# Kernel optimization log

Measured on AMD Instinct MI355X. Metric: run time of the kernel, lower is better.

The kernel has to match this reference:

```python
import jax, jax.numpy as jnp
import numpy as np

EMB = 1024
HEADS = 16
HEAD_SIZE = EMB // HEADS


def setup_inputs() -> dict:
    key = jax.random.key(0)
    ks = jax.random.split(key, 10)
    s = 1.0 / np.sqrt(EMB)
    return {
        "x": jax.random.normal(ks[0], (2, 2048, EMB), dtype=jnp.float32),
        "ln_gamma": jnp.ones((EMB,), jnp.float32),
        "ln_beta": jnp.zeros((EMB,), jnp.float32),
        "Wq": jax.random.normal(ks[1], (EMB, EMB), jnp.float32) * s,
        "bq": jnp.zeros((EMB,), jnp.float32),
        "Wk": jax.random.normal(ks[2], (EMB, EMB), jnp.float32) * s,
        "bk": jnp.zeros((EMB,), jnp.float32),
        "Wv": jax.random.normal(ks[3], (EMB, EMB), jnp.float32) * s,
        "bv": jnp.zeros((EMB,), jnp.float32),
        "Wo": jax.random.normal(ks[4], (EMB, EMB), jnp.float32) * s,
        "bo": jnpps if False else jnp.zeros((EMB,), jnp.float32),
    }


def _layernorm(x, gamma, beta, eps=1e-5):
    mu = jnp.mean(x, axis=-1, keepdims=True)
    var = jnp.mean(jnp.square(x - mu), axis=-1, keepdims=True)
    return (x - mu) * jax.lax.rsqrt(var + eps) * gamma + beta


def reference(x, ln_gamma, ln_beta, Wq, bq, Wk, bk, Wv, bv, Wo, bo):
    B, L, D = x.shape
    h = _layernorm(x, ln_gamma, ln_beta)
    # projections -> [B, H, L, hd]
    def split_heads(t):
        return t.reshape(B, L, HEADS, HEAD_SIZE).transpose(0, 2, 1, 3)
    q = split_heads(h @ Wq.T + bq)
    k = split_heads(h @ Wk.T + bk)
    v = split_heads(h @ Wv.T + bv)
    scale = HEAD_SIZE ** (-0.5)
    w = jnp.einsum("bhqd,bhkd->bhqk", q, k) * scale  # [B,H,L,L]
    w = jax.nn.softmax(w, axis=-1)
    o = jnp.einsum("bhqk,bhkd->bhqd", w, v)
    o = o.transpose(0, 2, 1, 3).reshape(B, L, D)
    o = o @ Wo.T + bo
    return x + o
```

## Files before the change

kernel.cpp:

```cpp
#include <hip/hip_runtime.h>
#include <math.h>

#define B_   2
#define L_   2048
#define EMB_ 1024
#define H_   16
#define HD_  64
#define M_   (B_ * L_)
#define KSPLIT 4
#define LOG2E 1.44269504088896f

typedef __bf16 bf16x8 __attribute__((ext_vector_type(8)));
typedef __bf16 bf16x4 __attribute__((ext_vector_type(4)));
typedef __bf16 bf16x2 __attribute__((ext_vector_type(2)));
typedef float floatx16 __attribute__((ext_vector_type(16)));
typedef unsigned int uintx2 __attribute__((ext_vector_type(2)));

typedef __attribute__((address_space(1))) const void GV;
typedef __attribute__((address_space(3))) void LV;

#define MFMA32(a, b, c) __builtin_amdgcn_mfma_f32_32x32x16_bf16((a), (b), (c), 0, 0, 0)

#if __has_builtin(__builtin_amdgcn_exp2f)
#define EXP2(x) __builtin_amdgcn_exp2f(x)
#else
#define EXP2(x) exp2f(x)
#endif

#define SWZ(row) ((((row) & 7) ^ (((row) >> 3) & 3)))

__device__ __forceinline__ int pkbf(float a, float b) {
#if __has_builtin(__builtin_amdgcn_cvt_pk_bf16_f32)
    union { bf16x2 v; int i; } u;
    u.v = __builtin_amdgcn_cvt_pk_bf16_f32(a, b);
    return u.i;
#else
    union { __bf16 h[2]; int i; } u;
    u.h[0] = (__bf16)a; u.h[1] = (__bf16)b;
    return u.i;
#endif
}

__global__ __launch_bounds__(256) void cvt_w_kernel(
        const float* __restrict__ s0, const float* __restrict__ s1,
        const float* __restrict__ s2, const float* __restrict__ s3,
        __bf16* __restrict__ d0, __bf16* __restrict__ d1,
        __bf16* __restrict__ d2, __bf16* __restrict__ d3) {
    int z = blockIdx.y;
    const float* s = (z == 0) ? s0 : (z == 1) ? s1 : (z == 2) ? s2 : s3;
    __bf16* d = (z == 0) ? d0 : (z == 1) ? d1 : (z == 2) ? d2 : d3;
    size_t base = (size_t)(blockIdx.x * 256 + threadIdx.x) * 16;
#pragma unroll
    for (int j = 0; j < 4; ++j) {
        float4 f = *(const float4*)(s + base + j * 4);
        bf16x4 t;
        t[0] = (__bf16)f.x; t[1] = (__bf16)f.y; t[2] = (__bf16)f.z; t[3] = (__bf16)f.w;
        *(bf16x4*)(d + base + j * 4) = t;
    }
}

__global__ __launch_bounds__(256) void ln_kernel(
        const float* __restrict__ x, const float* __restrict__ gamma,
        const float* __restrict__ beta, __bf16* __restrict__ h) {
    int row = blockIdx.x;
    int tid = threadIdx.x;
    const float* xr = x + (size_t)row * EMB_;
    float4 v = *(const float4*)(xr + tid * 4);
    float s  = v.x + v.y + v.z + v.w;
    float ss = v.x * v.x + v.y * v.y + v.z * v.z + v.w * v.w;
    for (int off = 32; off; off >>= 1) {
        s  += __shfl_down(s, off, 64);
        ss += __shfl_down(ss, off, 64);
    }
    __shared__ float s1[4], s2[4];
    int wid = tid >> 6;
    if ((tid & 63) == 0) { s1[wid] = s; s2[wid] = ss; }
    __syncthreads();
    if (tid == 0) {
        float a = s1[0] + s1[1] + s1[2] + s1[3];
        float b = s2[0] + s2[1] + s2[2] + s2[3];
        float mu = a / EMB_;
        float var = b / EMB_ - mu * mu;
        s1[0] = mu;
        s2[0] = rsqrtf(var + 1e-5f);
    }
    __syncthreads();
    float mu = s1[0], rstd = s2[0];
    float4 g4 = *(const float4*)(gamma + tid * 4);
    float4 b4 = *(const float4*)(beta + tid * 4);
    bf16x4 o;
    o[0] = (__bf16)((v.x - mu) * rstd * g4.x + b4.x);
    o[1] = (__bf16)((v.y - mu) * rstd * g4.y + b4.y);
    o[2] = (__bf16)((v.z - mu) * rstd * g4.z + b4.z);
    o[3] = (__bf16)((v.w - mu) * rstd * g4.w + b4.w);
    *(bf16x4*)(h + (size_t)row * EMB_ + tid * 4) = o;
}

__device__ __forceinline__ void stage_tile128(const __bf16* gbase, __bf16* lds,
                                              int wave, int lane) {
    int srow = lane >> 3;
    int gch0 = lane & 7;
#pragma unroll
    for (int s = 0; s < 4; ++s) {
        int seg = wave * 4 + s;
        int row = seg * 8 + srow;
        int g = gch0 ^ SWZ(row);
        __builtin_amdgcn_global_load_lds(
            (GV*)(gbase + (size_t)row * EMB_ + g * 8),
            (LV*)(lds + seg * 512 + lane * 8), 16, 0, 0);
    }
}

__global__ __launch_bounds__(256) void gemm_qkv_mfma(
        const __bf16* __restrict__ A, const __bf16* __restrict__ W,
        const float* __restrict__ bq, const float* __restrict__ bk,
        const float* __restrict__ bv,
        __bf16* __restrict__ Qo, __bf16* __restrict__ Ko,
        __bf16* __restrict__ Vto) {
    __shared__ __bf16 As[128 * 64];
    __shared__ __bf16 Bs[128 * 64];
    int tid = threadIdx.x, wave = tid >> 6, lane = tid & 63;
    int wm = wave >> 1, wn = wave & 1;
    int quad = lane >> 5, lq = lane & 31;
    int bm = blockIdx.y * 128, bn = blockIdx.x * 128;

    floatx16 acc[2][2];
#pragma unroll
    for (int i = 0; i < 2; ++i)
#pragma unroll
        for (int j = 0; j < 2; ++j)
#pragma unroll
            for (int r = 0; r < 16; ++r) acc[i][j][r] = 0.f;

    for (int k0 = 0; k0 < EMB_; k0 += 64) {
        __syncthreads();
        stage_tile128(A + (size_t)bm * EMB_ + k0, As, wave, lane);
        stage_tile128(W + (size_t)bn * EMB_ + k0, Bs, wave, lane);
        __syncthreads();
#pragma unroll
        for (int s = 0; s < 4; ++s) {
            int g = 2 * s + quad;
            int r0 = wm * 64 + lq, r1 = r0 + 32;
            int c0 = wn * 64 + lq, c1 = c0 + 32;
            bf16x8 a0 = *(const bf16x8*)&As[r0 * 64 + ((g ^ SWZ(r0)) * 8)];
            bf16x8 a1 = *(const bf16x8*)&As[r1 * 64 + ((g ^ SWZ(r1)) * 8)];
            bf16x8 b0 = *(const bf16x8*)&Bs[c0 * 64 + ((g ^ SWZ(c0)) * 8)];
            bf16x8 b1 = *(const bf16x8*)&Bs[c1 * 64 + ((g ^ SWZ(c1)) * 8)];
            acc[0][0] = MFMA32(a0, b0, acc[0][0]);
            acc[0][1] = MFMA32(a0, b1, acc[0][1]);
            acc[1][0] = MFMA32(a1, b0, acc[1][0]);
            acc[1][1] = MFMA32(a1, b1, acc[1][1]);
        }
    }

#pragma unroll
    for (int mb = 0; mb < 2; ++mb) {
#pragma unroll
        for (int nb = 0; nb < 2; ++nb) {
            int col = bn + wn * 64 + nb * 32 + lq;
            int z = col >> 10;
            int cc = col & 1023;
            float bv_ = (z == 0) ? bq[cc] : (z == 1) ? bk[cc] : bv[cc];
            if (z < 2) {
                __bf16* dst = (z == 0) ? Qo : Ko;
                float qs = (z == 0) ? 0.125f * LOG2E : 1.0f;
#pragma unroll
                for (int r = 0; r < 16; ++r) {
                    int row = bm + wm * 64 + mb * 32 + (r & 3) + 8 * (r >> 2) + 4 * quad;
                    dst[(size_t)row * EMB_ + cc] = (__bf16)((acc[mb][nb][r] + bv_) * qs);
                }
            } else {
                int hh = cc >> 6, d = cc & 63;
#pragma unroll
                for (int rb = 0; rb < 4; ++rb) {
                    int row = bm + wm * 64 + mb * 32 + 8 * rb + 4 * quad;
                    int b = row >> 11, l = row & (L_ - 1);
                    bf16x4 t;
#pragma unroll
                    for (int a = 0; a < 4; ++a) t[a] = (__bf16)(acc[mb][nb][4 * rb + a] + bv_);
                    *(bf16x4*)(Vto + ((size_t)(b * H_ + hh) * HD_ + d) * L_ + l) = t;
                }
            }
        }
    }
}

template <int SEGS>
__device__ __forceinline__ void stage_tile(const __bf16* gbase, __bf16* lds,
                                           int wave, int lane) {
    int srow = lane >> 3;
    int gch0 = lane & 7;
#pragma unroll
    for (int s = 0; s < SEGS; ++s) {
        int seg = wave * SEGS + s;
        int row = seg * 8 + srow;
        int g = gch0 ^ SWZ(row);
        __builtin_amdgcn_global_load_lds(
            (GV*)(gbase + (size_t)row * EMB_ + g * 8),
            (LV*)(lds + seg * 512 + lane * 8), 16, 0, 0);
    }
}

__global__ __launch_bounds__(256) void gemm_out_mfma(
        const __bf16* __restrict__ A, const __bf16* __restrict__ W,
        const float* __restrict__ bias, const float* __restrict__ x,
        float* __restrict__ out) {
    __shared__ __bf16 As[64 * 64];
    __shared__ __bf16 Bs[128 * 64];
    int tid = threadIdx.x, wave = tid >> 6, lane = tid & 63;
    int quad = lane >> 5, lq = lane & 31;
    int bm = blockIdx.y * 64, bn = blockIdx.x * 128;

    floatx16 acc[2];
#pragma unroll
    for (int i = 0; i < 2; ++i)
#pragma unroll
        for (int r = 0; r < 16; ++r) acc[i][r] = 0.f;

    for (int k0 = 0; k0 < EMB_; k0 += 64) {
        __syncthreads();
        stage_tile<2>(A + (size_t)bm * EMB_ + k0, As, wave, lane);
        stage_tile<4>(W + (size_t)bn * EMB_ + k0, Bs, wave, lane);
        __syncthreads();
#pragma unroll
        for (int s = 0; s < 4; ++s) {
            int g = 2 * s + quad;
            int r0 = lq, r1 = lq + 32;
            int c = wave * 32 + lq;
            bf16x8 a0 = *(const bf16x8*)&As[r0 * 64 + ((g ^ SWZ(r0)) * 8)];
            bf16x8 a1 = *(const bf16x8*)&As[r1 * 64 + ((g ^ SWZ(r1)) * 8)];
            bf16x8 b  = *(const bf16x8*)&Bs[c * 64 + ((g ^ SWZ(c)) * 8)];
            acc[0] = MFMA32(a0, b, acc[0]);
            acc[1] = MFMA32(a1, b, acc[1]);
        }
    }

    int col = bn + wave * 32 + lq;
    float bv_ = bias[col];
#pragma unroll
    for (int mb = 0; mb < 2; ++mb) {
#pragma unroll
        for (int r = 0; r < 16; ++r) {
            size_t row = bm + mb * 32 + (r & 3) + 8 * (r >> 2) + 4 * quad;
            out[row * EMB_ + col] = acc[mb][r] + bv_ + x[row * EMB_ + col];
        }
    }
}

__global__ __launch_bounds__(512, 4) void attn_mfma(
        const __bf16* __restrict__ Q,
        const __bf16* __restrict__ K,
        const __bf16* __restrict__ Vt,
        __bf16* __restrict__ Op,
        float* __restrict__ Lp) {
    __shared__ __bf16 Ks[2][64 * 64];
    __shared__ __bf16 Vs[2][64 * 64];

    int tid = threadIdx.x, wave = tid >> 6, lane = tid & 63;
    int quad = lane >> 5, lq = lane & 31;
    int bh = blockIdx.x;
    int ks = blockIdx.z;
    int b = bh >> 4, h = bh & 15;
    int q0 = blockIdx.y * 256 + wave * 32;
    const size_t tok0 = (size_t)b * L_;

    const __bf16* Kb = K + tok0 * EMB_ + h * HD_;
    const __bf16* Vb = Vt + (size_t)bh * HD_ * L_;

    bf16x8 qf[4];
    {
        const __bf16* qp = Q + (tok0 + q0 + lq) * EMB_ + h * HD_ + quad * 8;
#pragma unroll
        for (int s = 0; s < 4; ++s) qf[s] = *(const bf16x8*)(qp + s * 16);
    }

    floatx16 oacc[2];
#pragma unroll
    for (int j = 0; j < 2; ++j)
#pragma unroll
        for (int r = 0; r < 16; ++r) oacc[j][r] = 0.f;
    float lacc = 0.f;

    int srow = lane >> 3, gch0 = lane & 7;

    auto stage = [&](int buf, int kt) {
        int row = wave * 8 + srow;
        int g = gch0 ^ SWZ(row);
        __builtin_amdgcn_global_load_lds(
            (GV*)(Kb + (size_t)(kt + row) * EMB_ + g * 8),
            (LV*)(&Ks[buf][wave * 512 + lane * 8]), 16, 0, 0);
        __builtin_amdgcn_global_load_lds(
            (GV*)(Vb + (size_t)row * L_ + kt + g * 8),
            (LV*)(&Vs[buf][wave * 512 + lane * 8]), 16, 0, 0);
    };

    auto compute = [&](int buf) {
#pragma unroll
        for (int nb = 0; nb < 2; ++nb) {
            int krow = nb * 32 + lq;
            bf16x8 kf[4];
#pragma unroll
            for (int s = 0; s < 4; ++s)
                kf[s] = *(const bf16x8*)&Ks[buf][krow * 64 + (((2 * s + quad) ^ SWZ(krow)) * 8)];

            floatx16 sacc;
#pragma unroll
            for (int r = 0; r < 16; ++r) sacc[r] = 0.f;
            __builtin_amdgcn_s_setprio(1);
#pragma unroll
            for (int s = 0; s < 4; ++s) sacc = MFMA32(kf[s], qf[s], sacc);
            __builtin_amdgcn_s_setprio(0);

            int P[8];
            float lsum = 0.f;
#pragma unroll
            for (int t = 0; t < 8; ++t) {
                float pa = EXP2(sacc[2 * t]);
                float pb = EXP2(sacc[2 * t + 1]);
                lsum += pa + pb;
                P[t] = pkbf(pa, pb);
            }
            lacc += lsum;
            union { int i[4]; bf16x8 v; } bf0, bf1;
#if __has_builtin(__builtin_amdgcn_permlane32_swap)
            {
                uintx2 r;
                r = __builtin_amdgcn_permlane32_swap((unsigned)P[0], (unsigned)P[2], false, false);
                bf0.i[0] = (int)r[0]; bf0.i[2] = (int)r[1];
                r = __builtin_amdgcn_permlane32_swap((unsigned)P[1], (unsigned)P[3], false, false);
                bf0.i[1] = (int)r[0]; bf0.i[3] = (int)r[1];
                r = __builtin_amdgcn_permlane32_swap((unsigned)P[4], (unsigned)P[6], false, false);
                bf1.i[0] = (int)r[0]; bf1.i[2] = (int)r[1];
                r = __builtin_amdgcn_permlane32_swap((unsigned)P[5], (unsigned)P[7], false, false);
                bf1.i[1] = (int)r[0]; bf1.i[3] = (int)r[1];
            }
#else
            int X[8];
#pragma unroll
            for (int t = 0; t < 8; ++t) X[t] = __shfl_xor(P[t], 32, 64);
            bf0.i[0] = quad ? X[2] : P[0];
            bf0.i[1] = quad ? X[3] : P[1];
            bf0.i[2] = quad ? P[2] : X[0];
            bf0.i[3] = quad ? P[3] : X[1];
            bf1.i[0] = quad ? X[6] : P[4];
            bf1.i[1] = quad ? X[7] : P[5];
            bf1.i[2] = quad ? P[6] : X[4];
            bf1.i[3] = quad ? P[7] : X[5];
#endif

            __builtin_amdgcn_s_setprio(1);
#pragma unroll
            for (int half = 0; half < 2; ++half) {
                int t = 2 * nb + half;
#pragma unroll
                for (int db = 0; db < 2; ++db) {
                    int drow = db * 32 + lq;
                    bf16x8 vf = *(const bf16x8*)&Vs[buf][drow * 64 + (((2 * t + quad) ^ SWZ(drow)) * 8)];
                    oacc[db] = MFMA32(vf, half ? bf1.v : bf0.v, oacc[db]);
                }
            }
            __builtin_amdgcn_s_setprio(0);
        }
    };

    const int kt0 = ks * (L_ / KSPLIT);
    const int NT = (L_ / KSPLIT) / 64;

    stage(0, kt0);
    for (int t = 0; t < NT; ++t) {
        __syncthreads();
        if (t + 1 < NT) stage((t + 1) & 1, kt0 + (t + 1) * 64);
        compute(t & 1);
    }

    {
        float l = lacc + __shfl_xor(lacc, 32, 64);
        if (lane < 32)
            Lp[((size_t)ks * 32 + bh) * L_ + q0 + lane] = l;
    }
#pragma unroll
    for (int db = 0; db < 2; ++db)
#pragma unroll
        for (int r = 0; r < 16; ++r) {
            int dp = db * 32 + (r & 3) + 8 * (r >> 2) + 4 * quad;
            Op[((size_t)(ks * 32 + bh) * HD_ + dp) * L_ + q0 + lq] =
                (__bf16)oacc[db][r];
        }
}

__global__ __launch_bounds__(256) void combine_kernel(
        const __bf16* __restrict__ Op, const float* __restrict__ Lp,
        __bf16* __restrict__ Ob) {
    __shared__ float lrl[64];
    __shared__ __bf16 T[64][72];
    int t = threadIdx.x;
    int qt = blockIdx.x * 64;
    int bh = blockIdx.y;
    int b = bh >> 4, h = bh & 15;

    if (t < 64) {
        float l = 0.f;
#pragma unroll
        for (int ks = 0; ks < KSPLIT; ++ks)
            l += Lp[((size_t)ks * 32 + bh) * L_ + qt + t];
        lrl[t] = 1.0f / l;
    }
    __syncthreads();

#pragma unroll
    for (int cc = 0; cc < 2; ++cc) {
        int id = t + cc * 256;
        int d = id >> 3, q8 = (id & 7) * 8;
        float acc[8];
#pragma unroll
        for (int j = 0; j < 8; ++j) acc[j] = 0.f;
#pragma unroll
        for (int ks = 0; ks < KSPLIT; ++ks) {
            bf16x8 v = *(const bf16x8*)(Op + ((size_t)(ks * 32 + bh) * HD_ + d) * L_ + qt + q8);
#pragma unroll
            for (int j = 0; j < 8; ++j) acc[j] += (float)v[j];
        }
#pragma unroll
        for (int j = 0; j < 8; ++j)
            T[q8 + j][d] = (__bf16)(acc[j] * lrl[q8 + j]);
    }
    __syncthreads();

#pragma unroll
    for (int cc = 0; cc < 2; ++cc) {
        int id = t + cc * 256;
        int tl = id >> 3, dc = (id & 7) * 8;
        bf16x8 v = *(const bf16x8*)&T[tl][dc];
        *(bf16x8*)(Ob + ((size_t)b * L_ + qt + tl) * EMB_ + h * HD_ + dc) = v;
    }
}

extern "C" void kernel_launch(void* const* d_in, const int* in_sizes, int n_in,
                              void* d_out, int out_size, void* d_ws, size_t ws_size,
                              hipStream_t stream) {
    const float* x     = (const float*)d_in[0];
    const float* gamma = (const float*)d_in[1];
    const float* beta  = (const float*)d_in[2];
    const float* Wq    = (const float*)d_in[3];
    const float* bq    = (const float*)d_in[4];
    const float* Wk    = (const float*)d_in[5];
    const float* bk    = (const float*)d_in[6];
    const float* Wv    = (const float*)d_in[7];
    const float* bv    = (const float*)d_in[8];
    const float* Wo    = (const float*)d_in[9];
    const float* bo    = (const float*)d_in[10];
    float* out = (float*)d_out;

    const size_t SLAB = (size_t)M_ * EMB_;
    const size_t WSLAB = (size_t)EMB_ * EMB_;
    char* ws = (char*)d_ws;
    __bf16* hb    = (__bf16*)ws;                      ws += SLAB * 2;
    __bf16* Qb    = (__bf16*)ws;                      ws += SLAB * 2;
    __bf16* Kb    = (__bf16*)ws;                      ws += SLAB * 2;
    __bf16* Vtb   = (__bf16*)ws;                      ws += SLAB * 2;
    __bf16* Wqkvb = (__bf16*)ws;                      ws += 3 * WSLAB * 2;
    __bf16* Wob   = (__bf16*)ws;                      ws += WSLAB * 2;
    __bf16* Op    = (__bf16*)ws;                      ws += (size_t)KSPLIT * SLAB * 2;
    float*  Lp    = (float*)ws;                       ws += (size_t)KSPLIT * 32 * L_ * 4;
    __bf16* Ob    = hb;

    cvt_w_kernel<<<dim3(256, 4), 256, 0, stream>>>(
        Wq, Wk, Wv, Wo, Wqkvb, Wqkvb + WSLAB, Wqkvb + 2 * WSLAB, Wob);
    ln_kernel<<<M_, 256, 0, stream>>>(x, gamma, beta, hb);
    gemm_qkv_mfma<<<dim3(3 * EMB_ / 128, M_ / 128), 256, 0, stream>>>(
        hb, Wqkvb, bq, bk, bv, Qb, Kb, Vtb);
    attn_mfma<<<dim3(B_ * H_, L_ / 256, KSPLIT), 512, 0, stream>>>(Qb, Kb, Vtb, Op, Lp);
    combine_kernel<<<dim3(L_ / 64, B_ * H_), 256, 0, stream>>>(Op, Lp, Ob);
    gemm_out_mfma<<<dim3(EMB_ / 128, M_ / 64), 256, 0, stream>>>(Ob, Wob, bo, x, out);
}
```

Before: 197.9 us.

## Merge LN and weight cast into one launch, widen attention KV tiles, halve KSPLIT

After: 220.7 us. +11.5%, slower.

```diff
diff --git a/kernel.cpp b/kernel.cpp
--- a/kernel.cpp
+++ b/kernel.cpp
@@ -7,7 +7,7 @@
 #define H_   16
 #define HD_  64
 #define M_   (B_ * L_)
-#define KSPLIT 4
+#define KSPLIT 2
 #define LOG2E 1.44269504088896f
 
 typedef __bf16 bf16x8 __attribute__((ext_vector_type(8)));
@@ -41,29 +41,31 @@
 #endif
 }
 
-__global__ __launch_bounds__(256) void cvt_w_kernel(
+__global__ __launch_bounds__(256) void prep_kernel(
+        const float* __restrict__ x, const float* __restrict__ gamma,
+        const float* __restrict__ beta, __bf16* __restrict__ h,
         const float* __restrict__ s0, const float* __restrict__ s1,
         const float* __restrict__ s2, const float* __restrict__ s3,
         __bf16* __restrict__ d0, __bf16* __restrict__ d1,
         __bf16* __restrict__ d2, __bf16* __restrict__ d3) {
-    int z = blockIdx.y;
-    const float* s = (z == 0) ? s0 : (z == 1) ? s1 : (z == 2) ? s2 : s3;
-    __bf16* d = (z == 0) ? d0 : (z == 1) ? d1 : (z == 2) ? d2 : d3;
-    size_t base = (size_t)(blockIdx.x * 256 + threadIdx.x) * 16;
-#pragma unroll
-    for (int j = 0; j < 4; ++j) {
-        float4 f = *(const float4*)(s + base + j * 4);
-        bf16x4 t;
-        t[0] = (__bf16)f.x; t[1] = (__bf16)f.y; t[2] = (__bf16)f.z; t[3] = (__bf16)f.w;
-        *(bf16x4*)(d + base + j * 4) = t;
-    }
-}
-
-__global__ __launch_bounds__(256) void ln_kernel(
-        const float* __restrict__ x, const float* __restrict__ gamma,
-        const float* __restrict__ beta, __bf16* __restrict__ h) {
-    int row = blockIdx.x;
+    int bid = blockIdx.x;
     int tid = threadIdx.x;
+    if (bid >= M_) {
+        int wb = bid - M_;
+        int z = wb >> 8;
+        const float* s = (z == 0) ? s0 : (z == 1) ? s1 : (z == 2) ? s2 : s3;
+        __bf16* d = (z == 0) ? d0 : (z == 1) ? d1 : (z == 2) ? d2 : d3;
+        size_t base = (size_t)((wb & 255) * 256 + tid) * 16;
+#pragma unroll
+        for (int j = 0; j < 4; ++j) {
+            float4 f = *(const float4*)(s + base + j * 4);
+            bf16x4 t;
+            t[0] = (__bf16)f.x; t[1] = (__bf16)f.y; t[2] = (__bf16)f.z; t[3] = (__bf16)f.w;
+            *(bf16x4*)(d + base + j * 4) = t;
+        }
+        return;
+    }
+    int row = bid;
     const float* xr = x + (size_t)row * EMB_;
     float4 v = *(const float4*)(xr + tid * 4);
     float s  = v.x + v.y + v.z + v.w;
@@ -72,20 +74,20 @@
         s  += __shfl_down(s, off, 64);
         ss += __shfl_down(ss, off, 64);
     }
-    __shared__ float s1[4], s2[4];
+    __shared__ float s1_[4], s2_[4];
     int wid = tid >> 6;
-    if ((tid & 63) == 0) { s1[wid] = s; s2[wid] = ss; }
+    if ((tid & 63) == 0) { s1_[wid] = s; s2_[wid] = ss; }
     __syncthreads();
     if (tid == 0) {
-        float a = s1[0] + s1[1] + s1[2] + s1[3];
-        float b = s2[0] + s2[1] + s2[2] + s2[3];
+        float a = s1_[0] + s1_[1] + s1_[2] + s1_[3];
+        float b = s2_[0] + s2_[1] + s2_[2] + s2_[3];
         float mu = a / EMB_;
         float var = b / EMB_ - mu * mu;
-        s1[0] = mu;
-        s2[0] = rsqrtf(var + 1e-5f);
+        s1_[0] = mu;
+        s2_[0] = rsqrtf(var + 1e-5f);
     }
     __syncthreads();
-    float mu = s1[0], rstd = s2[0];
+    float mu = s1_[0], rstd = s2_[0];
     float4 g4 = *(const float4*)(gamma + tid * 4);
     float4 b4 = *(const float4*)(beta + tid * 4);
     bf16x4 o;
@@ -253,8 +255,8 @@
         const __bf16* __restrict__ Vt,
         __bf16* __restrict__ Op,
         float* __restrict__ Lp) {
-    __shared__ __bf16 Ks[2][64 * 64];
-    __shared__ __bf16 Vs[2][64 * 64];
+    __shared__ __bf16 Ks[2][2][64 * 64];
+    __shared__ __bf16 Vs[2][2][64 * 64];
 
     int tid = threadIdx.x, wave = tid >> 6, lane = tid & 63;
     int quad = lane >> 5, lq = lane & 31;
@@ -286,90 +288,96 @@
     auto stage = [&](int buf, int kt) {
         int row = wave * 8 + srow;
         int g = gch0 ^ SWZ(row);
-        __builtin_amdgcn_global_load_lds(
-            (GV*)(Kb + (size_t)(kt + row) * EMB_ + g * 8),
-            (LV*)(&Ks[buf][wave * 512 + lane * 8]), 16, 0, 0);
-        __builtin_amdgcn_global_load_lds(
-            (GV*)(Vb + (size_t)row * L_ + kt + g * 8),
-            (LV*)(&Vs[buf][wave * 512 + lane * 8]), 16, 0, 0);
+#pragma unroll
+        for (int kh = 0; kh < 2; ++kh) {
+            __builtin_amdgcn_global_load_lds(
+                (GV*)(Kb + (size_t)(kt + kh * 64 + row) * EMB_ + g * 8),
+                (LV*)(&Ks[buf][kh][wave * 512 + lane * 8]), 16, 0, 0);
+            __builtin_amdgcn_global_load_lds(
+                (GV*)(Vb + (size_t)row * L_ + kt + kh * 64 + g * 8),
+                (LV*)(&Vs[buf][kh][wave * 512 + lane * 8]), 16, 0, 0);
+        }
     };
 
     auto compute = [&](int buf) {
 #pragma unroll
-        for (int nb = 0; nb < 2; ++nb) {
-            int krow = nb * 32 + lq;
-            bf16x8 kf[4];
-#pragma unroll
-            for (int s = 0; s < 4; ++s)
-                kf[s] = *(const bf16x8*)&Ks[buf][krow * 64 + (((2 * s + quad) ^ SWZ(krow)) * 8)];
-
-            floatx16 sacc;
-#pragma unroll
-            for (int r = 0; r < 16; ++r) sacc[r] = 0.f;
-            __builtin_amdgcn_s_setprio(1);
-#pragma unroll
-            for (int s = 0; s < 4; ++s) sacc = MFMA32(kf[s], qf[s], sacc);
-            __builtin_amdgcn_s_setprio(0);
-
-            int P[8];
-            float lsum = 0.f;
-#pragma unroll
-            for (int t = 0; t < 8; ++t) {
-                float pa = EXP2(sacc[2 * t]);
-                float pb = EXP2(sacc[2 * t + 1]);
-                lsum += pa + pb;
-                P[t] = pkbf(pa, pb);
+        for (int kh = 0; kh < 2; ++kh) {
+#pragma unroll
+            for (int nb = 0; nb < 2; ++nb) {
+                int krow = nb * 32 + lq;
+                bf16x8 kf[4];
+#pragma unroll
+                for (int s = 0; s < 4; ++s)
+                    kf[s] = *(const bf16x8*)&Ks[buf][kh][krow * 64 + (((2 * s + quad) ^ SWZ(krow)) * 8)];
+
+                floatx16 sacc;
+#pragma unroll
+                for (int r = 0; r < 16; ++r) sacc[r] = 0.f;
+                __builtin_amdgcn_s_setprio(1);
+#pragma unroll
+                for (int s = 0; s < 4; ++s) sacc = MFMA32(kf[s], qf[s], sacc);
+                __builtin_amdgcn_s_setprio(0);
+
+                int P[8];
+                float lsum = 0.f;
+#pragma unroll
+                for (int t = 0; t < 8; ++t) {
+                    float pa = EXP2(sacc[2 * t]);
+                    float pb = EXP2(sacc[2 * t + 1]);
+                    lsum += pa + pb;
+                    P[t] = pkbf(pa, pb);
+                }
+                lacc += lsum;
+                union { int i[4]; bf16x8 v; } bf0, bf1;
+#if __has_builtin(__builtin_amdgcn_permlane32_swap)
+                {
+                    uintx2 r;
+                    r = __builtin_amdgcn_permlane32_swap((unsigned)P[0], (unsigned)P[2], false, false);
+                    bf0.i[0] = (int)r[0]; bf0.i[2] = (int)r[1];
+                    r = __builtin_amdgcn_permlane32_swap((unsigned)P[1], (unsigned)P[3], false, false);
+                    bf0.i[1] = (int)r[0]; bf0.i[3] = (int)r[1];
+                    r = __builtin_amdgcn_permlane32_swap((unsigned)P[4], (unsigned)P[6], false, false);
+                    bf1.i[0] = (int)r[0]; bf1.i[2] = (int)r[1];
+                    r = __builtin_amdgcn_permlane32_swap((unsigned)P[5], (unsigned)P[7], false, false);
+                    bf1.i[1] = (int)r[0]; bf1.i[3] = (int)r[1];
+                }
+#else
+                int X[8];
+#pragma unroll
+                for (int t = 0; t < 8; ++t) X[t] = __shfl_xor(P[t], 32, 64);
+                bf0.i[0] = quad ? X[2] : P[0];
+                bf0.i[1] = quad ? X[3] : P[1];
+                bf0.i[2] = quad ? P[2] : X[0];
+                bf0.i[3] = quad ? P[3] : X[1];
+                bf1.i[0] = quad ? X[6] : P[4];
+                bf1.i[1] = quad ? X[7] : P[5];
+                bf1.i[2] = quad ? P[6] : X[4];
+                bf1.i[3] = quad ? P[7] : X[5];
+#endif
+
+                __builtin_amdgcn_s_setprio(1);
+#pragma unroll
+                for (int half = 0; half < 2; ++half) {
+                    int t = 2 * nb + half;
+#pragma unroll
+                    for (int db = 0; db < 2; ++db) {
+                        int drow = db * 32 + lq;
+                        bf16x8 vf = *(const bf16x8*)&Vs[buf][kh][drow * 64 + (((2 * t + quad) ^ SWZ(drow)) * 8)];
+                        oacc[db] = MFMA32(vf, half ? bf1.v : bf0.v, oacc[db]);
+                    }
+                }
+                __builtin_amdgcn_s_setprio(0);
             }
-            lacc += lsum;
-            union { int i[4]; bf16x8 v; } bf0, bf1;
-#if __has_builtin(__builtin_amdgcn_permlane32_swap)
-            {
-                uintx2 r;
-                r = __builtin_amdgcn_permlane32_swap((unsigned)P[0], (unsigned)P[2], false, false);
-                bf0.i[0] = (int)r[0]; bf0.i[2] = (int)r[1];
-                r = __builtin_amdgcn_permlane32_swap((unsigned)P[1], (unsigned)P[3], false, false);
-                bf0.i[1] = (int)r[0]; bf0.i[3] = (int)r[1];
-                r = __builtin_amdgcn_permlane32_swap((unsigned)P[4], (unsigned)P[6], false, false);
-                bf1.i[0] = (int)r[0]; bf1.i[2] = (int)r[1];
-                r = __builtin_amdgcn_permlane32_swap((unsigned)P[5], (unsigned)P[7], false, false);
-                bf1.i[1] = (int)r[0]; bf1.i[3] = (int)r[1];
-            }
-#else
-            int X[8];
-#pragma unroll
-            for (int t = 0; t < 8; ++t) X[t] = __shfl_xor(P[t], 32, 64);
-            bf0.i[0] = quad ? X[2] : P[0];
-            bf0.i[1] = quad ? X[3] : P[1];
-            bf0.i[2] = quad ? P[2] : X[0];
-            bf0.i[3] = quad ? P[3] : X[1];
-            bf1.i[0] = quad ? X[6] : P[4];
-            bf1.i[1] = quad ? X[7] : P[5];
-            bf1.i[2] = quad ? P[6] : X[4];
-            bf1.i[3] = quad ? P[7] : X[5];
-#endif
-
-            __builtin_amdgcn_s_setprio(1);
-#pragma unroll
-            for (int half = 0; half < 2; ++half) {
-                int t = 2 * nb + half;
-#pragma unroll
-                for (int db = 0; db < 2; ++db) {
-                    int drow = db * 32 + lq;
-                    bf16x8 vf = *(const bf16x8*)&Vs[buf][drow * 64 + (((2 * t + quad) ^ SWZ(drow)) * 8)];
-                    oacc[db] = MFMA32(vf, half ? bf1.v : bf0.v, oacc[db]);
-                }
-            }
-            __builtin_amdgcn_s_setprio(0);
         }
     };
 
     const int kt0 = ks * (L_ / KSPLIT);
-    const int NT = (L_ / KSPLIT) / 64;
+    const int NT = (L_ / KSPLIT) / 128;
 
     stage(0, kt0);
     for (int t = 0; t < NT; ++t) {
         __syncthreads();
-        if (t + 1 < NT) stage((t + 1) & 1, kt0 + (t + 1) * 64);
+        if (t + 1 < NT) stage((t + 1) & 1, kt0 + (t + 1) * 128);
         compute(t & 1);
     }
 
@@ -464,9 +472,9 @@
     float*  Lp    = (float*)ws;                       ws += (size_t)KSPLIT * 32 * L_ * 4;
     __bf16* Ob    = hb;
 
-    cvt_w_kernel<<<dim3(256, 4), 256, 0, stream>>>(
+    prep_kernel<<<M_ + 1024, 256, 0, stream>>>(
+        x, gamma, beta, hb,
         Wq, Wk, Wv, Wo, Wqkvb, Wqkvb + WSLAB, Wqkvb + 2 * WSLAB, Wob);
-    ln_kernel<<<M_, 256, 0, stream>>>(x, gamma, beta, hb);
     gemm_qkv_mfma<<<dim3(3 * EMB_ / 128, M_ / 128), 256, 0, stream>>>(
         hb, Wqkvb, bq, bk, bv, Qb, Kb, Vtb);
     attn_mfma<<<dim3(B_ * H_, L_ / 256, KSPLIT), 512, 0, stream>>>(Qb, Kb, Vtb, Op, Lp);
```
